# Kernel optimization log

Measured on AMD Instinct MI355X. Metric: run time of the kernel, lower is better.

Reference implementation:

```python
import jax, jax.numpy as jnp
import numpy as np

N_EXPERTS = 8
TOP_K = 2


def setup_inputs() -> dict:
    key = jax.random.key(0)
    ks = jax.random.split(key, 5)
    B, T, D, E, H = 4, 2048, 1024, N_EXPERTS, 2730  # H = int(2*D*4/3)
    x = jax.random.normal(ks[0], (B, T, D), dtype=jnp.float32)
    gate_w = jax.random.normal(ks[1], (E, D), dtype=jnp.float32) * 0.02
    w1 = jax.random.normal(ks[2], (E, H, D), dtype=jnp.float32) * 0.02
    w3 = jax.random.normal(ks[3], (E, H, D), dtype=jnp.float32) * 0.02
    w2 = jax.random.normal(ks[4], (E, D, H), dtype=jnp.float32) * 0.02
    return {"x": x, "gate_w": gate_w, "w1": w1, "w3": w3, "w2": w2}


def reference(x, gate_w, w1, w3, w2):
    B, T, D = x.shape
    E = gate_w.shape[0]
    x_flat = x.reshape(-1, D)  # [N, D], N = B*T
    N = x_flat.shape[0]

    # Router: top-k over softmax probabilities, renormalized over selected experts
    logits = x_flat @ gate_w.T                      # [N, E]
    probs = jax.nn.softmax(logits, axis=-1)         # [N, E]
    top_v, top_i = jax.lax.top_k(probs, TOP_K)      # [N, K]
    top_v = top_v / jnp.sum(top_v, axis=-1, keepdims=True)

    # Dense combine weights [N, E]: weight of expert e for each token (0 if not selected).
    # top_k indices are distinct per token, so scatter-add equals scatter-set here.
    combine = jnp.zeros((N, E), dtype=x.dtype).at[
        jnp.arange(N)[:, None], top_i
    ].add(top_v)

    # Weighted combine of SwiGLU experts (loop over small fixed expert count).
    out = jnp.zeros_like(x_flat)
    for e in range(E):
        gate = jax.nn.silu(x_flat @ w1[e].T)        # [N, H]
        up = x_flat @ w3[e].T                       # [N, H]
        y = (gate * up) @ w2[e].T                   # [N, D]
        out = out + combine[:, e:e + 1] * y

    aux_loss = jnp.asarray(0.0, dtype=x.dtype)  # use_aux_loss=False / eval mode
    return out.reshape(B, T, D), aux_loss
```

## Files before the change

### kernel.cpp

```cpp
#include <hip/hip_runtime.h>
#include <hip/hip_bf16.h>

#define N_TOK 8192
#define D_DIM 1024
#define E_NUM 8
#define H_DIM 2730
#define HP    2816
#define NP    5632
#define NROWS (N_TOK*2)
#define MAXTILES 136

typedef __bf16 bf16;
typedef __bf16 bf16x8 __attribute__((ext_vector_type(8)));
typedef __bf16 bf16x4 __attribute__((ext_vector_type(4)));
typedef float  f32x4  __attribute__((ext_vector_type(4)));

__device__ __forceinline__ void gload_lds16(const bf16* g, bf16* l) {
  __builtin_amdgcn_global_load_lds((const __attribute__((address_space(1))) void*)g,
                                   (__attribute__((address_space(3))) void*)l, 16, 0, 0);
}
#define VMCNT(n) asm volatile("s_waitcnt vmcnt(" #n ")" ::: "memory")
#define LGKM0()  asm volatile("s_waitcnt lgkmcnt(0)" ::: "memory")
#define BAR() __builtin_amdgcn_s_barrier()

__global__ void conv13_kernel(const float* __restrict__ w1, const float* __restrict__ w3,
                              bf16* __restrict__ Bp) {
  int i = blockIdx.x * blockDim.x + threadIdx.x;
  if (i >= E_NUM * NP * 128) return;
  int c8 = i & 127;
  int r  = (i >> 7) % NP;
  int e  = i / (NP * 128);
  int hc = ((r >> 5) << 4) + (r & 15);
  bf16x8 o;
  if (hc < H_DIM) {
    const float* s = (((r >> 4) & 1) ? w3 : w1) + ((long)e * H_DIM + hc) * D_DIM + c8 * 8;
    float4 a0 = ((const float4*)s)[0], a1 = ((const float4*)s)[1];
    o[0]=(bf16)a0.x; o[1]=(bf16)a0.y; o[2]=(bf16)a0.z; o[3]=(bf16)a0.w;
    o[4]=(bf16)a1.x; o[5]=(bf16)a1.y; o[6]=(bf16)a1.z; o[7]=(bf16)a1.w;
  } else {
    #pragma unroll
    for (int j = 0; j < 8; j++) o[j] = (bf16)0.f;
  }
  ((bf16x8*)Bp)[i] = o;
}

__global__ void conv_w2_kernel(const float* __restrict__ src, bf16* __restrict__ dst) {
  int i = blockIdx.x * blockDim.x + threadIdx.x;
  if (i >= E_NUM * D_DIM * (HP / 8)) return;
  int c8 = i % (HP / 8);
  int row = i / (HP / 8);
  int c = c8 * 8;
  const float* s = src + (long)row * H_DIM + c;
  bf16x8 o;
  #pragma unroll
  for (int j = 0; j < 8; j++) o[j] = (c + j < H_DIM) ? (bf16)s[j] : (bf16)0.f;
  ((bf16x8*)dst)[i] = o;
}

__global__ void router_kernel(const float* __restrict__ x, const float* __restrict__ gw,
                              int* __restrict__ topi, float* __restrict__ topw,
                              int* __restrict__ counts) {
  int t = blockIdx.x * (blockDim.x >> 6) + (threadIdx.x >> 6);
  int lane = threadIdx.x & 63;
  if (t >= N_TOK) return;
  const float* xr = x + (long)t * D_DIM;
  float acc[E_NUM];
  #pragma unroll
  for (int e = 0; e < E_NUM; e++) acc[e] = 0.f;
  for (int j = 0; j < D_DIM / 64; j++) {
    float xv = xr[j * 64 + lane];
    #pragma unroll
    for (int e = 0; e < E_NUM; e++) acc[e] += xv * gw[e * D_DIM + j * 64 + lane];
  }
  #pragma unroll
  for (int e = 0; e < E_NUM; e++) {
    float v = acc[e];
    #pragma unroll
    for (int s = 32; s > 0; s >>= 1) v += __shfl_xor(v, s, 64);
    acc[e] = v;
  }
  if (lane == 0) {
    int b0 = -1, b1 = -1; float v0 = -1e30f, v1 = -1e30f;
    #pragma unroll
    for (int e = 0; e < E_NUM; e++) {
      float v = acc[e];
      if (v > v0) { v1 = v0; b1 = b0; v0 = v; b0 = e; }
      else if (v > v1) { v1 = v; b1 = e; }
    }
    float w0 = 1.f / (1.f + expf(v1 - v0));
    topi[t * 2] = b0; topi[t * 2 + 1] = b1;
    topw[t * 2] = w0; topw[t * 2 + 1] = 1.f - w0;
    atomicAdd(&counts[b0], 1); atomicAdd(&counts[b1], 1);
  }
}

__global__ void tiles_kernel(const int* __restrict__ counts, int* __restrict__ offs,
                             int* __restrict__ tlist) {
  if (threadIdx.x == 0) {
    int s = 0, idx = 0;
    for (int e = 0; e < E_NUM; e++) {
      offs[e] = s;
      int ne = counts[e];
      s += ne;
      int nt = (ne + 127) >> 7;
      for (int t = 0; t < nt; t++) tlist[idx++] = (e << 8) | t;
    }
    offs[E_NUM] = s;
    for (; idx < MAXTILES; idx++) tlist[idx] = -1;
  }
}

__global__ void scatter_kernel(const int* __restrict__ topi, const float* __restrict__ topw,
                               const int* __restrict__ offs, int* __restrict__ cursor,
                               int* __restrict__ rowmap, float* __restrict__ roww,
                               int* __restrict__ rowoftok) {
  int i = blockIdx.x * blockDim.x + threadIdx.x;
  if (i >= NROWS) return;
  int e = topi[i];
  int pos = atomicAdd(&cursor[e], 1);
  int row = offs[e] + pos;
  rowmap[row] = i >> 1;
  roww[row] = topw[i];
  rowoftok[i] = row;
}

__global__ void gather_kernel(const float* __restrict__ x, const int* __restrict__ rowmap,
                              bf16* __restrict__ Xg) {
  int r = blockIdx.x * (blockDim.x >> 6) + (threadIdx.x >> 6);
  int lane = threadIdx.x & 63;
  if (r >= NROWS) return;
  int t = rowmap[r];
  const float4* src = (const float4*)(x + (long)t * D_DIM);
  bf16x4* dst = (bf16x4*)(Xg + (long)r * D_DIM);
  #pragma unroll
  for (int j = 0; j < 4; j++) {
    float4 v = src[j * 64 + lane];
    bf16x4 o; o[0]=(bf16)v.x; o[1]=(bf16)v.y; o[2]=(bf16)v.z; o[3]=(bf16)v.w;
    dst[j * 64 + lane] = o;
  }
}

__global__ void combine_kernel(const bf16* __restrict__ y, const int* __restrict__ rowoftok,
                               const float* __restrict__ topw, float* __restrict__ out) {
  int t = blockIdx.x * (blockDim.x >> 6) + (threadIdx.x >> 6);
  int lane = threadIdx.x & 63;
  if (t >= N_TOK) return;
  int r0 = rowoftok[t * 2], r1 = rowoftok[t * 2 + 1];
  float w0 = topw[t * 2], w1 = topw[t * 2 + 1];
  const bf16x8* y0 = (const bf16x8*)(y + (long)r0 * D_DIM);
  const bf16x8* y1 = (const bf16x8*)(y + (long)r1 * D_DIM);
  float* o = out + (long)t * D_DIM;
  #pragma unroll
  for (int j = 0; j < 2; j++) {
    bf16x8 a = y0[j * 64 + lane], b = y1[j * 64 + lane];
    float4 v0, v1;
    v0.x = w0*(float)a[0] + w1*(float)b[0]; v0.y = w0*(float)a[1] + w1*(float)b[1];
    v0.z = w0*(float)a[2] + w1*(float)b[2]; v0.w = w0*(float)a[3] + w1*(float)b[3];
    v1.x = w0*(float)a[4] + w1*(float)b[4]; v1.y = w0*(float)a[5] + w1*(float)b[5];
    v1.z = w0*(float)a[6] + w1*(float)b[6]; v1.w = w0*(float)a[7] + w1*(float)b[7];
    float4* op = (float4*)(o + (j * 64 + lane) * 8);
    op[0] = v0; op[1] = v1;
  }
}


#define G1_STAGE(SB, T) do { \
    _Pragma("unroll") for (int L_ = 0; L_ < 2; L_++) \
      gload_lds16(aS[L_] + (T) * 32, smem + (SB) + w * 1024 + L_ * 512); \
    _Pragma("unroll") for (int L_ = 0; L_ < 4; L_++) \
      gload_lds16(bS[L_] + (T) * 32, smem + (SB) + 4096 + w * 2048 + L_ * 512); \
  } while (0)

#define G1_READ0(SB) do { \
    _Pragma("unroll") for (int m_ = 0; m_ < 4; m_++) \
      af[m_] = *(const bf16x8*)&smem[(SB) + (wr * 64 + m_ * 16 + fr) * 32 + qp]; \
    _Pragma("unroll") for (int q_ = 0; q_ < 4; q_++) \
      bf0[q_] = *(const bf16x8*)&smem[(SB) + 4096 + (wc * 128 + q_ * 16 + fr) * 32 + qp]; \
  } while (0)

#define G1_MFMA0() do { __builtin_amdgcn_s_setprio(1); \
    _Pragma("unroll") for (int m_ = 0; m_ < 4; m_++) \
    _Pragma("unroll") for (int q_ = 0; q_ < 4; q_++) \
      acc[m_][q_] = __builtin_amdgcn_mfma_f32_16x16x32_bf16(af[m_], bf0[q_], acc[m_][q_], 0, 0, 0); \
    __builtin_amdgcn_s_setprio(0); } while (0)

#define G1_READ1(SB) do { \
    _Pragma("unroll") for (int q_ = 0; q_ < 4; q_++) \
      bf1[q_] = *(const bf16x8*)&smem[(SB) + 4096 + (wc * 128 + (q_ + 4) * 16 + fr) * 32 + qp]; \
  } while (0)

#define G1_MFMA1() do { __builtin_amdgcn_s_setprio(1); \
    _Pragma("unroll") for (int m_ = 0; m_ < 4; m_++) \
    _Pragma("unroll") for (int q_ = 0; q_ < 4; q_++) \
      acc[m_][q_ + 4] = __builtin_amdgcn_mfma_f32_16x16x32_bf16(af[m_], bf1[q_], acc[m_][q_ + 4], 0, 0, 0); \
    __builtin_amdgcn_s_setprio(0); } while (0)

__global__ __launch_bounds__(256, 2) void gemm1_kernel(
    const bf16* __restrict__ Xg, const bf16* __restrict__ Bp,
    const int* __restrict__ counts, const int* __restrict__ offs,
    const int* __restrict__ tlist, bf16* __restrict__ h) {
  int bid = blockIdx.x;
  int tile = bid / 22, col = bid - tile * 22;
  int te = tlist[tile];
  if (te < 0) return;
  int e = te >> 8, tm = te & 255;
  int ne = counts[e];
  int row_base = offs[e];
  int n0 = col * 256;

  __shared__ bf16 smem[3 * 12288];
  int tid = threadIdx.x, w = tid >> 6, lane = tid & 63;
  int wr = w >> 1, wc = w & 1;
  int fr = lane & 15, hi = lane >> 4;
  int qp = (hi ^ ((fr >> 1) & 3)) * 8;
  int srcq = ((lane & 3) ^ ((lane >> 3) & 3)) * 8;
  int srow = lane >> 2;

  f32x4 acc[4][8];
  #pragma unroll
  for (int m = 0; m < 4; m++)
    #pragma unroll
    for (int q = 0; q < 8; q++) acc[m][q] = (f32x4)0.f;

  const bf16* Bpe = Bp + (long)e * NP * D_DIM;
  const bf16* aS[2];
  const bf16* bS[4];
  #pragma unroll
  for (int L = 0; L < 2; L++) {
    int ra = row_base + min(tm * 128 + w * 32 + L * 16 + srow, ne - 1);
    aS[L] = Xg + (long)ra * D_DIM + srcq;
  }
  #pragma unroll
  for (int L = 0; L < 4; L++) {
    int rb = n0 + w * 64 + L * 16 + srow;
    bS[L] = Bpe + (long)rb * D_DIM + srcq;
  }

  bf16x8 af[4], bf0[4], bf1[4];

  G1_STAGE(0, 0); G1_STAGE(12288, 1);
  VMCNT(6); BAR();

  int sbC = 0, sbS = 24576;
  for (int t = 0; t < 30; t++) {
    G1_READ0(sbC);
    G1_STAGE(sbS, t + 2);
    BAR();
    G1_MFMA0();
    G1_READ1(sbC);
    G1_MFMA1();
    LGKM0(); VMCNT(6); BAR();
    sbC += 12288; if (sbC > 24576) sbC = 0;
    sbS += 12288; if (sbS > 24576) sbS = 0;
  }
  { G1_READ0(sbC); BAR(); G1_MFMA0(); G1_READ1(sbC); G1_MFMA1(); LGKM0(); VMCNT(0); BAR();
    sbC += 12288; if (sbC > 24576) sbC = 0; }
  { G1_READ0(sbC); G1_MFMA0(); G1_READ1(sbC); G1_MFMA1(); }

  int crow4 = hi * 4;
  #pragma unroll
  for (int m = 0; m < 4; m++)
    #pragma unroll
    for (int j = 0; j < 4; j++) {
      int rloc = tm * 128 + wr * 64 + m * 16 + crow4 + j;
      if (rloc < ne) {
        long hrow = (long)(row_base + rloc) * HP;
        #pragma unroll
        for (int p = 0; p < 4; p++) {
          int col2 = (n0 >> 1) + wc * 64 + p * 16 + fr;
          float g = acc[m][2 * p][j], u = acc[m][2 * p + 1][j];
          h[hrow + col2] = (bf16)((g / (1.f + __expf(-g))) * u);
        }
      }
    }
}

#define G2_STAGE(SB, T) do { \
    _Pragma("unroll") for (int L_ = 0; L_ < 2; L_++) \
      gload_lds16(aS[L_] + (T) * 32, smem2 + (SB) + w * 1024 + L_ * 512); \
    _Pragma("unroll") for (int L_ = 0; L_ < 2; L_++) \
      gload_lds16(bS[L_] + (T) * 32, smem2 + (SB) + 4096 + w * 1024 + L_ * 512); \
  } while (0)

#define G2_READ(SB) do { \
    _Pragma("unroll") for (int m_ = 0; m_ < 4; m_++) \
      af[m_] = *(const bf16x8*)&smem2[(SB) + (wr * 64 + m_ * 16 + fr) * 32 + qp]; \
    _Pragma("unroll") for (int n_ = 0; n_ < 4; n_++) \
      bfr[n_] = *(const bf16x8*)&smem2[(SB) + 4096 + (wc * 64 + n_ * 16 + fr) * 32 + qp]; \
  } while (0)

#define G2_MFMA() do { __builtin_amdgcn_s_setprio(1); \
    _Pragma("unroll") for (int m_ = 0; m_ < 4; m_++) \
    _Pragma("unroll") for (int n_ = 0; n_ < 4; n_++) \
      acc[m_][n_] = __builtin_amdgcn_mfma_f32_16x16x32_bf16(af[m_], bfr[n_], acc[m_][n_], 0, 0, 0); \
    __builtin_amdgcn_s_setprio(0); } while (0)

__global__ __launch_bounds__(256, 3) void gemm2_kernel(
    const bf16* __restrict__ h, const bf16* __restrict__ w2b,
    const int* __restrict__ counts, const int* __restrict__ offs,
    const int* __restrict__ tlist, bf16* __restrict__ y) {
  int bid = blockIdx.x;
  int tile = bid >> 3, col = bid & 7;
  int te = tlist[tile];
  if (te < 0) return;
  int e = te >> 8, tm = te & 255;
  int ne = counts[e];
  int row_base = offs[e];
  int n0 = col * 128;

  __shared__ bf16 smem2[3 * 8192];
  int tid = threadIdx.x, w = tid >> 6, lane = tid & 63;
  int wr = w >> 1, wc = w & 1;
  int fr = lane & 15, hi = lane >> 4;
  int qp = (hi ^ ((fr >> 1) & 3)) * 8;
  int srcq = ((lane & 3) ^ ((lane >> 3) & 3)) * 8;
  int srow = lane >> 2;

  f32x4 acc[4][4];
  #pragma unroll
  for (int m = 0; m < 4; m++)
    #pragma unroll
    for (int n = 0; n < 4; n++) acc[m][n] = (f32x4)0.f;

  const bf16* w2e = w2b + (long)e * D_DIM * HP;
  const bf16* aS[2];
  const bf16* bS[2];
  #pragma unroll
  for (int L = 0; L < 2; L++) {
    int ra = row_base + min(tm * 128 + w * 32 + L * 16 + srow, ne - 1);
    aS[L] = h + (long)ra * HP + srcq;
    int rb = n0 + w * 32 + L * 16 + srow;
    bS[L] = w2e + (long)rb * HP + srcq;
  }

  bf16x8 af[4], bfr[4];

  G2_STAGE(0, 0); G2_STAGE(8192, 1);
  VMCNT(4); BAR();

  int sbC = 0, sbS = 16384;
  for (int t = 0; t < 86; t++) {
    G2_READ(sbC);
    G2_STAGE(sbS, t + 2);
    BAR();
    G2_MFMA();
    LGKM0(); VMCNT(4); BAR();
    sbC += 8192; if (sbC > 16384) sbC = 0;
    sbS += 8192; if (sbS > 16384) sbS = 0;
  }
  { G2_READ(sbC); BAR(); G2_MFMA(); LGKM0(); VMCNT(0); BAR();
    sbC += 8192; if (sbC > 16384) sbC = 0; }
  { G2_READ(sbC); G2_MFMA(); }

  int crow4 = hi * 4;
  #pragma unroll
  for (int m = 0; m < 4; m++)
    #pragma unroll
    for (int j = 0; j < 4; j++) {
      int rloc = tm * 128 + wr * 64 + m * 16 + crow4 + j;
      if (rloc < ne) {
        long yrow = (long)(row_base + rloc) * D_DIM;
        #pragma unroll
        for (int n = 0; n < 4; n++) {
          int col2 = n0 + wc * 64 + n * 16 + fr;
          y[yrow + col2] = (bf16)acc[m][n][j];
        }
      }
    }
}

extern "C" void kernel_launch(void* const* d_in, const int* in_sizes, int n_in,
                              void* d_out, int out_size, void* d_ws, size_t ws_size,
                              hipStream_t stream) {
  const float* x  = (const float*)d_in[0];
  const float* gw = (const float*)d_in[1];
  const float* w1 = (const float*)d_in[2];
  const float* w3 = (const float*)d_in[3];
  const float* w2 = (const float*)d_in[4];
  float* out = (float*)d_out;

  char* ws = (char*)d_ws;
  int*   counts   = (int*)(ws);
  int*   cursor   = (int*)(ws + 64);
  int*   offs     = (int*)(ws + 128);
  int*   tlist    = (int*)(ws + 192);
  int*   topi     = (int*)(ws + 2048);
  float* topw     = (float*)(ws + 2048 + 65536);
  int*   rowmap   = (int*)(ws + 2048 + 131072);
  float* roww     = (float*)(ws + 2048 + 196608);
  int*   rowoftok = (int*)(ws + 2048 + 262144);
  char*  big      = ws + 2048 + 327680;
  bf16* Bp   = (bf16*)big;
  bf16* w2b  = (bf16*)big;
  bf16* Xg   = Bp + (size_t)E_NUM * NP * D_DIM;
  bf16* hbuf = Xg + (size_t)NROWS * D_DIM;
  bf16* ybuf = Xg;

  hipMemsetAsync((char*)d_out + (size_t)(out_size - 1) * sizeof(float), 0, sizeof(float), stream);
  hipMemsetAsync(ws, 0, 256, stream);

  int nbp = E_NUM * NP * 128;
  conv13_kernel<<<(nbp + 255) / 256, 256, 0, stream>>>(w1, w3, Bp);

  router_kernel<<<N_TOK / 4, 256, 0, stream>>>(x, gw, topi, topw, counts);
  tiles_kernel<<<1, 64, 0, stream>>>(counts, offs, tlist);
  scatter_kernel<<<(NROWS + 255) / 256, 256, 0, stream>>>(topi, topw, offs, cursor, rowmap, roww, rowoftok);
  gather_kernel<<<NROWS / 4, 256, 0, stream>>>(x, rowmap, Xg);

  gemm1_kernel<<<MAXTILES * 22, 256, 0, stream>>>(Xg, Bp, counts, offs, tlist, hbuf);

  int w2n = E_NUM * D_DIM * (HP / 8);
  conv_w2_kernel<<<(w2n + 255) / 256, 256, 0, stream>>>(w2, w2b);

  gemm2_kernel<<<MAXTILES * 8, 256, 0, stream>>>(hbuf, w2b, counts, offs, tlist, ybuf);
  combine_kernel<<<N_TOK / 4, 256, 0, stream>>>(ybuf, rowoftok, topw, out);
}
```

Baseline: 744.7 us.

## Reshape MoE GEMM tiles: 256-row tiles for gemm1, 256-col tiles for gemm2

Gemm1 now uses 256-token row tiles with 128 packed weight columns, taken from a second tile list of 256-row groups per expert. Each wave owns a full 64-row slice, so weight columns are shared across more tokens. Gemm2 moves from 128x128 to 128x256 output tiles, with 8 accumulator columns per wave and two-phase LDS reads like gemm1, and occupancy drops from 3 to 2 blocks. The goal is to raise arithmetic intensity and cut repeated weight or activation loads, at the cost of more padding waste on partial 256-row tiles, fewer blocks, and higher register pressure in gemm2.

```diff
diff --git a/kernel.cpp b/kernel.cpp
--- a/kernel.cpp
+++ b/kernel.cpp
@@ -9,6 +9,7 @@
 #define NP    5632
 #define NROWS (N_TOK*2)
 #define MAXTILES 136
+#define MAXT256  72
 
 typedef __bf16 bf16;
 typedef __bf16 bf16x8 __attribute__((ext_vector_type(8)));
@@ -95,18 +96,21 @@
 }
 
 __global__ void tiles_kernel(const int* __restrict__ counts, int* __restrict__ offs,
-                             int* __restrict__ tlist) {
+                             int* __restrict__ tlist, int* __restrict__ tlist2) {
   if (threadIdx.x == 0) {
-    int s = 0, idx = 0;
+    int s = 0, idx = 0, idx2 = 0;
     for (int e = 0; e < E_NUM; e++) {
       offs[e] = s;
       int ne = counts[e];
       s += ne;
       int nt = (ne + 127) >> 7;
       for (int t = 0; t < nt; t++) tlist[idx++] = (e << 8) | t;
+      int nt2 = (ne + 255) >> 8;
+      for (int t = 0; t < nt2; t++) tlist2[idx2++] = (e << 8) | t;
     }
     offs[E_NUM] = s;
     for (; idx < MAXTILES; idx++) tlist[idx] = -1;
+    for (; idx2 < MAXT256; idx2++) tlist2[idx2] = -1;
   }
 }
 
@@ -165,17 +169,17 @@
 
 
 #define G1_STAGE(SB, T) do { \
+    _Pragma("unroll") for (int L_ = 0; L_ < 4; L_++) \
+      gload_lds16(aS[L_] + (T) * 32, smem + (SB) + w * 2048 + L_ * 512); \
     _Pragma("unroll") for (int L_ = 0; L_ < 2; L_++) \
-      gload_lds16(aS[L_] + (T) * 32, smem + (SB) + w * 1024 + L_ * 512); \
-    _Pragma("unroll") for (int L_ = 0; L_ < 4; L_++) \
-      gload_lds16(bS[L_] + (T) * 32, smem + (SB) + 4096 + w * 2048 + L_ * 512); \
+      gload_lds16(bS[L_] + (T) * 32, smem + (SB) + 8192 + w * 1024 + L_ * 512); \
   } while (0)
 
 #define G1_READ0(SB) do { \
     _Pragma("unroll") for (int m_ = 0; m_ < 4; m_++) \
-      af[m_] = *(const bf16x8*)&smem[(SB) + (wr * 64 + m_ * 16 + fr) * 32 + qp]; \
+      af[m_] = *(const bf16x8*)&smem[(SB) + (w * 64 + m_ * 16 + fr) * 32 + qp]; \
     _Pragma("unroll") for (int q_ = 0; q_ < 4; q_++) \
-      bf0[q_] = *(const bf16x8*)&smem[(SB) + 4096 + (wc * 128 + q_ * 16 + fr) * 32 + qp]; \
+      bf0[q_] = *(const bf16x8*)&smem[(SB) + 8192 + (q_ * 16 + fr) * 32 + qp]; \
   } while (0)
 
 #define G1_MFMA0() do { __builtin_amdgcn_s_setprio(1); \
@@ -186,7 +190,7 @@
 
 #define G1_READ1(SB) do { \
     _Pragma("unroll") for (int q_ = 0; q_ < 4; q_++) \
-      bf1[q_] = *(const bf16x8*)&smem[(SB) + 4096 + (wc * 128 + (q_ + 4) * 16 + fr) * 32 + qp]; \
+      bf1[q_] = *(const bf16x8*)&smem[(SB) + 8192 + ((q_ + 4) * 16 + fr) * 32 + qp]; \
   } while (0)
 
 #define G1_MFMA1() do { __builtin_amdgcn_s_setprio(1); \
@@ -198,19 +202,18 @@
 __global__ __launch_bounds__(256, 2) void gemm1_kernel(
     const bf16* __restrict__ Xg, const bf16* __restrict__ Bp,
     const int* __restrict__ counts, const int* __restrict__ offs,
-    const int* __restrict__ tlist, bf16* __restrict__ h) {
+    const int* __restrict__ tlist2, bf16* __restrict__ h) {
   int bid = blockIdx.x;
-  int tile = bid / 22, col = bid - tile * 22;
-  int te = tlist[tile];
+  int tile = bid / 44, col = bid - tile * 44;
+  int te = tlist2[tile];
   if (te < 0) return;
   int e = te >> 8, tm = te & 255;
   int ne = counts[e];
   int row_base = offs[e];
-  int n0 = col * 256;
+  int n0 = col * 128;
 
   __shared__ bf16 smem[3 * 12288];
   int tid = threadIdx.x, w = tid >> 6, lane = tid & 63;
-  int wr = w >> 1, wc = w & 1;
   int fr = lane & 15, hi = lane >> 4;
   int qp = (hi ^ ((fr >> 1) & 3)) * 8;
   int srcq = ((lane & 3) ^ ((lane >> 3) & 3)) * 8;
@@ -223,16 +226,16 @@
     for (int q = 0; q < 8; q++) acc[m][q] = (f32x4)0.f;
 
   const bf16* Bpe = Bp + (long)e * NP * D_DIM;
-  const bf16* aS[2];
-  const bf16* bS[4];
+  const bf16* aS[4];
+  const bf16* bS[2];
+  #pragma unroll
+  for (int L = 0; L < 4; L++) {
+    int ra = row_base + min(tm * 256 + w * 64 + L * 16 + srow, ne - 1);
+    aS[L] = Xg + (long)ra * D_DIM + srcq;
+  }
   #pragma unroll
   for (int L = 0; L < 2; L++) {
-    int ra = row_base + min(tm * 128 + w * 32 + L * 16 + srow, ne - 1);
-    aS[L] = Xg + (long)ra * D_DIM + srcq;
-  }
-  #pragma unroll
-  for (int L = 0; L < 4; L++) {
-    int rb = n0 + w * 64 + L * 16 + srow;
+    int rb = n0 + w * 32 + L * 16 + srow;
     bS[L] = Bpe + (long)rb * D_DIM + srcq;
   }
 
@@ -262,12 +265,12 @@
   for (int m = 0; m < 4; m++)
     #pragma unroll
     for (int j = 0; j < 4; j++) {
-      int rloc = tm * 128 + wr * 64 + m * 16 + crow4 + j;
+      int rloc = tm * 256 + w * 64 + m * 16 + crow4 + j;
       if (rloc < ne) {
         long hrow = (long)(row_base + rloc) * HP;
         #pragma unroll
         for (int p = 0; p < 4; p++) {
-          int col2 = (n0 >> 1) + wc * 64 + p * 16 + fr;
+          int col2 = (n0 >> 1) + p * 16 + fr;
           float g = acc[m][2 * p][j], u = acc[m][2 * p + 1][j];
           h[hrow + col2] = (bf16)((g / (1.f + __expf(-g))) * u);
         }
@@ -278,37 +281,48 @@
 #define G2_STAGE(SB, T) do { \
     _Pragma("unroll") for (int L_ = 0; L_ < 2; L_++) \
       gload_lds16(aS[L_] + (T) * 32, smem2 + (SB) + w * 1024 + L_ * 512); \
-    _Pragma("unroll") for (int L_ = 0; L_ < 2; L_++) \
-      gload_lds16(bS[L_] + (T) * 32, smem2 + (SB) + 4096 + w * 1024 + L_ * 512); \
-  } while (0)
-
-#define G2_READ(SB) do { \
+    _Pragma("unroll") for (int L_ = 0; L_ < 4; L_++) \
+      gload_lds16(bS[L_] + (T) * 32, smem2 + (SB) + 4096 + (L_ * 4 + w) * 512); \
+  } while (0)
+
+#define G2_READ0(SB) do { \
     _Pragma("unroll") for (int m_ = 0; m_ < 4; m_++) \
       af[m_] = *(const bf16x8*)&smem2[(SB) + (wr * 64 + m_ * 16 + fr) * 32 + qp]; \
     _Pragma("unroll") for (int n_ = 0; n_ < 4; n_++) \
-      bfr[n_] = *(const bf16x8*)&smem2[(SB) + 4096 + (wc * 64 + n_ * 16 + fr) * 32 + qp]; \
-  } while (0)
-
-#define G2_MFMA() do { __builtin_amdgcn_s_setprio(1); \
+      bf0[n_] = *(const bf16x8*)&smem2[(SB) + 4096 + (wc * 128 + n_ * 16 + fr) * 32 + qp]; \
+  } while (0)
+
+#define G2_MFMA0() do { __builtin_amdgcn_s_setprio(1); \
     _Pragma("unroll") for (int m_ = 0; m_ < 4; m_++) \
     _Pragma("unroll") for (int n_ = 0; n_ < 4; n_++) \
-      acc[m_][n_] = __builtin_amdgcn_mfma_f32_16x16x32_bf16(af[m_], bfr[n_], acc[m_][n_], 0, 0, 0); \
+      acc[m_][n_] = __builtin_amdgcn_mfma_f32_16x16x32_bf16(af[m_], bf0[n_], acc[m_][n_], 0, 0, 0); \
     __builtin_amdgcn_s_setprio(0); } while (0)
 
-__global__ __launch_bounds__(256, 3) void gemm2_kernel(
+#define G2_READ1(SB) do { \
+    _Pragma("unroll") for (int n_ = 0; n_ < 4; n_++) \
+      bf1[n_] = *(const bf16x8*)&smem2[(SB) + 4096 + (wc * 128 + (n_ + 4) * 16 + fr) * 32 + qp]; \
+  } while (0)
+
+#define G2_MFMA1() do { __builtin_amdgcn_s_setprio(1); \
+    _Pragma("unroll") for (int m_ = 0; m_ < 4; m_++) \
+    _Pragma("unroll") for (int n_ = 0; n_ < 4; n_++) \
+      acc[m_][n_ + 4] = __builtin_amdgcn_mfma_f32_16x16x32_bf16(af[m_], bf1[n_], acc[m_][n_ + 4], 0, 0, 0); \
+    __builtin_amdgcn_s_setprio(0); } while (0)
+
+__global__ __launch_bounds__(256, 2) void gemm2_kernel(
     const bf16* __restrict__ h, const bf16* __restrict__ w2b,
     const int* __restrict__ counts, const int* __restrict__ offs,
     const int* __restrict__ tlist, bf16* __restrict__ y) {
   int bid = blockIdx.x;
-  int tile = bid >> 3, col = bid & 7;
+  int tile = bid >> 2, col = bid & 3;
   int te = tlist[tile];
   if (te < 0) return;
   int e = te >> 8, tm = te & 255;
   int ne = counts[e];
   int row_base = offs[e];
-  int n0 = col * 128;
-
-  __shared__ bf16 smem2[3 * 8192];
+  int n0 = col * 256;
+
+  __shared__ bf16 smem2[3 * 12288];
   int tid = threadIdx.x, w = tid >> 6, lane = tid & 63;
   int wr = w >> 1, wc = w & 1;
   int fr = lane & 15, hi = lane >> 4;
@@ -316,41 +330,46 @@
   int srcq = ((lane & 3) ^ ((lane >> 3) & 3)) * 8;
   int srow = lane >> 2;
 
-  f32x4 acc[4][4];
+  f32x4 acc[4][8];
   #pragma unroll
   for (int m = 0; m < 4; m++)
     #pragma unroll
-    for (int n = 0; n < 4; n++) acc[m][n] = (f32x4)0.f;
+    for (int n = 0; n < 8; n++) acc[m][n] = (f32x4)0.f;
 
   const bf16* w2e = w2b + (long)e * D_DIM * HP;
   const bf16* aS[2];
-  const bf16* bS[2];
+  const bf16* bS[4];
   #pragma unroll
   for (int L = 0; L < 2; L++) {
     int ra = row_base + min(tm * 128 + w * 32 + L * 16 + srow, ne - 1);
     aS[L] = h + (long)ra * HP + srcq;
-    int rb = n0 + w * 32 + L * 16 + srow;
+  }
+  #pragma unroll
+  for (int L = 0; L < 4; L++) {
+    int rb = n0 + (L * 4 + w) * 16 + srow;
     bS[L] = w2e + (long)rb * HP + srcq;
   }
 
-  bf16x8 af[4], bfr[4];
-
-  G2_STAGE(0, 0); G2_STAGE(8192, 1);
-  VMCNT(4); BAR();
-
-  int sbC = 0, sbS = 16384;
+  bf16x8 af[4], bf0[4], bf1[4];
+
+  G2_STAGE(0, 0); G2_STAGE(12288, 1);
+  VMCNT(6); BAR();
+
+  int sbC = 0, sbS = 24576;
   for (int t = 0; t < 86; t++) {
-    G2_READ(sbC);
+    G2_READ0(sbC);
     G2_STAGE(sbS, t + 2);
     BAR();
-    G2_MFMA();
-    LGKM0(); VMCNT(4); BAR();
-    sbC += 8192; if (sbC > 16384) sbC = 0;
-    sbS += 8192; if (sbS > 16384) sbS = 0;
-  }
-  { G2_READ(sbC); BAR(); G2_MFMA(); LGKM0(); VMCNT(0); BAR();
-    sbC += 8192; if (sbC > 16384) sbC = 0; }
-  { G2_READ(sbC); G2_MFMA(); }
+    G2_MFMA0();
+    G2_READ1(sbC);
+    G2_MFMA1();
+    LGKM0(); VMCNT(6); BAR();
+    sbC += 12288; if (sbC > 24576) sbC = 0;
+    sbS += 12288; if (sbS > 24576) sbS = 0;
+  }
+  { G2_READ0(sbC); BAR(); G2_MFMA0(); G2_READ1(sbC); G2_MFMA1(); LGKM0(); VMCNT(0); BAR();
+    sbC += 12288; if (sbC > 24576) sbC = 0; }
+  { G2_READ0(sbC); G2_MFMA0(); G2_READ1(sbC); G2_MFMA1(); }
 
   int crow4 = hi * 4;
   #pragma unroll
@@ -361,8 +380,8 @@
       if (rloc < ne) {
         long yrow = (long)(row_base + rloc) * D_DIM;
         #pragma unroll
-        for (int n = 0; n < 4; n++) {
-          int col2 = n0 + wc * 64 + n * 16 + fr;
+        for (int n = 0; n < 8; n++) {
+          int col2 = n0 + wc * 128 + n * 16 + fr;
           y[yrow + col2] = (bf16)acc[m][n][j];
         }
       }
@@ -384,6 +403,7 @@
   int*   cursor   = (int*)(ws + 64);
   int*   offs     = (int*)(ws + 128);
   int*   tlist    = (int*)(ws + 192);
+  int*   tlist2   = (int*)(ws + 768);
   int*   topi     = (int*)(ws + 2048);
   float* topw     = (float*)(ws + 2048 + 65536);
   int*   rowmap   = (int*)(ws + 2048 + 131072);
@@ -403,15 +423,15 @@
   conv13_kernel<<<(nbp + 255) / 256, 256, 0, stream>>>(w1, w3, Bp);
 
   router_kernel<<<N_TOK / 4, 256, 0, stream>>>(x, gw, topi, topw, counts);
-  tiles_kernel<<<1, 64, 0, stream>>>(counts, offs, tlist);
+  tiles_kernel<<<1, 64, 0, stream>>>(counts, offs, tlist, tlist2);
   scatter_kernel<<<(NROWS + 255) / 256, 256, 0, stream>>>(topi, topw, offs, cursor, rowmap, roww, rowoftok);
   gather_kernel<<<NROWS / 4, 256, 0, stream>>>(x, rowmap, Xg);
 
-  gemm1_kernel<<<MAXTILES * 22, 256, 0, stream>>>(Xg, Bp, counts, offs, tlist, hbuf);
+  gemm1_kernel<<<MAXT256 * 44, 256, 0, stream>>>(Xg, Bp, counts, offs, tlist2, hbuf);
 
   int w2n = E_NUM * D_DIM * (HP / 8);
   conv_w2_kernel<<<(w2n + 255) / 256, 256, 0, stream>>>(w2, w2b);
 
-  gemm2_kernel<<<MAXTILES * 8, 256, 0, stream>>>(hbuf, w2b, counts, offs, tlist, ybuf);
+  gemm2_kernel<<<MAXTILES * 4, 256, 0, stream>>>(hbuf, w2b, counts, offs, tlist, ybuf);
   combine_kernel<<<N_TOK / 4, 256, 0, stream>>>(ybuf, rowoftok, topw, out);
 }
```

New measurement: 724.6 us. 1.03x faster.
